# Kernel optimization log

Hardware: AMD Instinct MI355X
Metric: run time of the kernel (lower is better)

## Reference

```python
import jax, jax.numpy as jnp
import numpy as np

B, Q, P = 8, 300, 5
RS, QS, CS, NC = 256, 768, 768, 396
HW = [64, 32, 16, 8]
POOL = [32, 16, 8, 4]
THR = 0.2


def _ln(x, g, b, eps=1e-5):
    m = x.mean(-1, keepdims=True)
    v = ((x - m) ** 2).mean(-1, keepdims=True)
    return (x - m) / jnp.sqrt(v + eps) * g + b


def _avgpool(x, oh, ow):
    # exact adaptive avg pool (output divides input)
    b, c, h, w = x.shape
    return x.reshape(b, c, oh, h // oh, ow, w // ow).mean((3, 5))


def setup_inputs() -> dict:
    key = jax.random.key(0)
    ks = jax.random.split(key, 40)
    inp = {}
    inp['pred_logits'] = jax.random.normal(ks[0], (B, Q, P), dtype=jnp.float32)
    inp['pred_boxes'] = jax.random.uniform(ks[1], (B, Q, 4), dtype=jnp.float32)
    inp['hs'] = jax.random.normal(ks[2], (B, Q, RS), dtype=jnp.float32)
    for s in range(4):
        inp[f'feat{s}'] = jax.random.normal(ks[3 + s], (B, 256, HW[s], HW[s]), dtype=jnp.float32)
        inp[f'pos{s}'] = jax.random.normal(ks[7 + s], (B, 256, HW[s], HW[s]), dtype=jnp.float32)
        inp[f'mask{s}'] = jax.random.bernoulli(ks[11 + s], 0.15, (B, HW[s], HW[s]))
        inp[f'convW{s}'] = jax.random.normal(ks[15 + s], (CS, 256), dtype=jnp.float32) * 0.02
        inp[f'convb{s}'] = jnp.zeros((CS,), jnp.float32)
        inp[f'lng{s}'] = jnp.ones((CS,), jnp.float32)
        inp[f'lnb{s}'] = jnp.zeros((CS,), jnp.float32)
    inp['learnable_query'] = jax.random.normal(ks[19], (P + 1, QS), dtype=jnp.float32)
    inp['Wq'] = jax.random.normal(ks[20], (RS, QS), dtype=jnp.float32) * 0.02
    inp['bq'] = jnp.zeros((QS,), jnp.float32)
    inp['qng'] = jnp.ones((QS,), jnp.float32)
    inp['qnb'] = jnp.zeros((QS,), jnp.float32)
    inp['W1'] = jax.random.normal(ks[21], (QS, QS), dtype=jnp.float32) * 0.02
    inp['b1'] = jnp.zeros((QS,), jnp.float32)
    inp['W2'] = jax.random.normal(ks[22], (QS, NC), dtype=jnp.float32) * 0.02
    inp['b2'] = jnp.zeros((NC,), jnp.float32)
    return inp


def _forward(pred_logits, pred_boxes, hs,
             feats, poss, masks, convWs, convbs, lngs, lnbs,
             learnable_query, Wq, bq, qng, qnb, W1, b1, W2, b2):
    del pred_boxes  # selected in the original but never used
    b = hs.shape[0]
    prob = jax.nn.sigmoid(pred_logits)                       # (B,Q,P)
    # per-prompt membership: logit_i > thr (implies max > thr)
    m = (prob > THR).astype(hs.dtype)                        # (B,Q,P)
    cnt = m.sum(1)                                           # (B,P)
    ssum = jnp.einsum('bqp,bqd->bpd', m, hs)                 # segment-sum over queries
    pooled = jnp.where(cnt[..., None] > 0,
                       ssum / jnp.maximum(cnt, 1.0)[..., None], 0.0)  # (B,P,RS)
    proj = pooled @ Wq + bq                                  # (B,P,QS)
    any_sel = jnp.any(prob.max(-1) > THR, axis=1)            # (B,)
    # if no query passed the global gate, prompt_hs is zeros WITHOUT projection
    prompt_hs = jnp.where(any_sel[:, None, None], proj, 0.0)
    prompt_query = learnable_query[1:] + prompt_hs           # (B,P,QS)
    cls_query = jnp.broadcast_to(learnable_query[0][None, None, :], (b, 1, QS))
    query_tokens = jnp.concatenate([cls_query, prompt_query], axis=1)
    query_tokens = _ln(query_tokens, qng, qnb)               # (B,P+1,QS)

    tokens = []
    for s in range(4):
        mask_f = masks[s][:, None, :, :].astype(feats[s].dtype)   # (B,1,H,W)
        x = (feats[s] + poss[s]) * (1.0 - mask_f)                 # masked_fill
        ctx = jnp.einsum('bchw,oc->bohw', x, convWs[s]) + convbs[s][None, :, None, None]
        p = _avgpool(ctx, POOL[s], POOL[s])
        mp = jnp.clip(_avgpool(1.0 - mask_f, POOL[s], POOL[s]), 1e-6, None)
        p = p / mp
        t = p.reshape(b, CS, -1).transpose(0, 2, 1)               # (B,T_s,CS)
        tokens.append(_ln(t, lngs[s], lnbs[s]))
    ctx_all = jnp.concatenate(tokens, axis=1)                     # (B,1360,CS)

    # encoder stand-in: fuse context into query tokens additively
    last = query_tokens + ctx_all.mean(1)[:, None, :]
    cls_logit = last[:, 0]
    prompt_logit = last[:, 1:].mean(1)
    h = jax.nn.relu((cls_logit + prompt_logit) @ W1 + b1)
    return h @ W2 + b2                                            # (B,NC)


def reference(pred_logits, pred_boxes, hs,
              feat0, pos0, mask0, convW0, convb0, lng0, lnb0,
              feat1, pos1, mask1, convW1, convb1, lng1, lnb1,
              feat2, pos2, mask2, convW2, convb2, lng2, lnb2,
              feat3, pos3, mask3, convW3, convb3, lng3, lnb3,
              learnable_query, Wq, bq, qng, qnb, W1, b1, W2, b2):
    return _forward(pred_logits, pred_boxes, hs,
                    [feat0, feat1, feat2, feat3],
                    [pos0, pos1, pos2, pos3],
                    [mask0, mask1, mask2, mask3],
                    [convW0, convW1, convW2, convW3],
                    [convb0, convb1, convb2, convb3],
                    [lng0, lng1, lng2, lng3],
                    [lnb0, lnb1, lnb2, lnb3],
                    learnable_query, Wq, bq, qng, qnb, W1, b1, W2, b2)
```

## Files before the change

kernel.cpp:

```cpp
#include <hip/hip_runtime.h>
#include <hip/hip_bf16.h>

#define Bn 8
#define Qn 300
#define Pn 5
#define RSn 256
#define QSn 768
#define NCn 396
#define MTOT 10880
#define THRL -1.3862943611198906f

typedef __attribute__((ext_vector_type(8))) short short8;
typedef __attribute__((ext_vector_type(4))) float float4v;

__device__ inline float wred(float v){
  #pragma unroll
  for (int off = 32; off; off >>= 1) v += __shfl_xor(v, off);
  return v;
}

__device__ __forceinline__ unsigned short f2bf(float f){
  union { float f; unsigned int u; } c; c.f = f;
  return (unsigned short)((c.u + 0x7FFF + ((c.u >> 16) & 1)) >> 16);
}

__global__ __launch_bounds__(256, 4) void k_front(
    const float* cw0, const float* cw1, const float* cw2, const float* cw3,
    short* Wswz, const int* __restrict__ mk0, int* det,
    const float* __restrict__ pl, const float* __restrict__ hs,
    float* pooled, int* flags, float* ctxsum, float* outz){
  int bx = blockIdx.x;
  int t = threadIdx.x;
  if (bx < 768){
    int s = bx / 192;
    int linear = (bx % 192)*256 + t;
    int q = linear & 63, n = linear >> 6;
    const float* src = (s==0)?cw0:(s==1)?cw1:(s==2)?cw2:cw3;
    float4 f = *(const float4*)(src + (size_t)n*256 + q*4);
    int kc = q >> 3, lk = (q >> 1) & 3, e0 = (q & 1)*4;
    short* dst = Wswz + ((size_t)(s*8 + kc))*24576 + lk*6144 + n*8 + e0;
    short4 sv;
    sv.x = (short)f2bf(f.x); sv.y = (short)f2bf(f.y);
    sv.z = (short)f2bf(f.z); sv.w = (short)f2bf(f.w);
    *(short4*)dst = sv;
    return;
  }
  if (bx == 768){
    __shared__ int r0[4], r1[4];
    const int* mm = mk0 + t*32;
    int d0 = 0, d1 = 0;
    #pragma unroll 8
    for (int i = 0; i < 32; ++i){
      int v = mm[i];
      d0 |= (v != 0 && v != 1);
      d1 |= (v != 0 && v != 0x3F800000);
    }
    unsigned long long bal0 = __ballot(d0), bal1 = __ballot(d1);
    int wid = t >> 6;
    if ((t & 63) == 0){ r0[wid] = (bal0 != 0ull); r1[wid] = (bal1 != 0ull); }
    __syncthreads();
    if (t == 0){
      det[0] = r0[0] | r0[1] | r0[2] | r0[3];
      det[1] = r1[0] | r1[1] | r1[2] | r1[3];
    }
    return;
  }
  if (bx >= 821){
    int idx = ((bx - 821)*256 + t)*4;
    if (idx < Bn*NCn) *(float4*)(outz + idx) = (float4){0.f,0.f,0.f,0.f};
    return;
  }
  if (bx >= 809){
    int idx = ((bx - 809)*256 + t)*4;
    *(float4*)(ctxsum + idx) = (float4){0.f,0.f,0.f,0.f};
    return;
  }
  __shared__ float msk[Qn];
  int bb = (bx - 769) / Pn, p = (bx - 769) % Pn;
  for (int q = t; q < Qn; q += 256)
    msk[q] = (pl[(bb*Qn + q)*Pn + p] > THRL) ? 1.f : 0.f;
  __syncthreads();
  const float* hb = hs + (size_t)bb*Qn*RSn + t;
  float sA[12];
  #pragma unroll
  for (int i = 0; i < 12; ++i) sA[i] = 0.f;
  float cnt = 0.f;
  for (int q0 = 0; q0 < Qn; q0 += 12){
    #pragma unroll
    for (int i = 0; i < 12; ++i){
      float m = msk[q0 + i];
      cnt += m;
      sA[i] = fmaf(m, hb[(size_t)(q0 + i)*RSn], sA[i]);
    }
  }
  float ssum = ((sA[0]+sA[1]) + (sA[2]+sA[3])) + ((sA[4]+sA[5]) + (sA[6]+sA[7]))
             + ((sA[8]+sA[9]) + (sA[10]+sA[11]));
  pooled[(bb*Pn + p)*RSn + t] = (cnt > 0.f) ? ssum / cnt : 0.f;
  if (t == 0) flags[bb*Pn + p] = (cnt > 0.f) ? 1 : 0;
}

__global__ __launch_bounds__(256, 3) void k_pgemm(
    const float* fe0, const float* po0, const void* ma0,
    const float* fe1, const float* po1, const void* ma1,
    const float* fe2, const float* po2, const void* ma2,
    const float* fe3, const float* po3, const void* ma3,
    const int* __restrict__ det, const short* __restrict__ Wswz,
    const float* cb0, const float* cb1, const float* cb2, const float* cb3,
    const float* lg0, const float* lb0, const float* lg1, const float* lb1,
    const float* lg2, const float* lb2, const float* lg3, const float* lb3,
    float* __restrict__ ctxsum,
    const float* __restrict__ lq, const float* __restrict__ Wq,
    const float* __restrict__ bq, const float* __restrict__ qng,
    const float* __restrict__ qnb, const float* __restrict__ pooled,
    const int* __restrict__ flags, float* qt){
  __shared__ short As[16*264];
  __shared__ float wls[16][4];
  __shared__ float scls[16], imls[16];
  __shared__ float lsum[4][16], lsq[4][16];
  __shared__ float pq[256];
  __shared__ float s1s[4], s2s[4];
  int blk = blockIdx.x;
  int t = threadIdx.x;

  if (blk >= 680){
    int qbx = blk - 680;
    int b = qbx / 6, j = qbx % 6;
    float v0 = lq[j*QSn + t], v1 = lq[j*QSn + t + 256], v2 = lq[j*QSn + t + 512];
    int any = flags[b*Pn] | flags[b*Pn+1] | flags[b*Pn+2] | flags[b*Pn+3] | flags[b*Pn+4];
    if (j > 0 && any){
      pq[t] = pooled[(b*Pn + (j-1))*RSn + t];
      __syncthreads();
      float a0 = 0.f, a1 = 0.f, a2 = 0.f;
      #pragma unroll 8
      for (int c = 0; c < RSn; ++c){
        float pv = pq[c];
        a0 = fmaf(pv, Wq[c*QSn + t      ], a0);
        a1 = fmaf(pv, Wq[c*QSn + t + 256], a1);
        a2 = fmaf(pv, Wq[c*QSn + t + 512], a2);
      }
      v0 += a0 + bq[t]; v1 += a1 + bq[t+256]; v2 += a2 + bq[t+512];
    }
    float sm = v0 + v1 + v2, sq = v0*v0 + v1*v1 + v2*v2;
    sm = wred(sm); sq = wred(sq);
    int wid = t >> 6, lane = t & 63;
    if (lane == 0){ s1s[wid] = sm; s2s[wid] = sq; }
    __syncthreads();
    float S  = s1s[0] + s1s[1] + s1s[2] + s1s[3];
    float SQ = s2s[0] + s2s[1] + s2s[2] + s2s[3];
    float mu = S * (1.f/QSn), var = SQ * (1.f/QSn) - mu*mu;
    float rs = rsqrtf(var + 1e-5f);
    float* o = qt + (b*6 + j)*QSn;
    o[t      ] = (v0 - mu)*rs*qng[t      ] + qnb[t      ];
    o[t + 256] = (v1 - mu)*rs*qng[t + 256] + qnb[t + 256];
    o[t + 512] = (v2 - mu)*rs*qng[t + 512] + qnb[t + 512];
    return;
  }

  int m0 = blk * 16;
  int s, H, OWlog, b0;
  const float *F, *Pp; const void* M;
  const float *CB, *LG, *LB;
  if (m0 < 8192){ s=0; F=fe0; Pp=po0; M=ma0; H=64; OWlog=5; b0=m0>>10;
                  CB=cb0; LG=lg0; LB=lb0; }
  else if (m0 < 10240){ s=1; F=fe1; Pp=po1; M=ma1; H=32; OWlog=4; b0=(m0-8192)>>8;
                  CB=cb1; LG=lg1; LB=lb1; }
  else if (m0 < 10752){ s=2; F=fe2; Pp=po2; M=ma2; H=16; OWlog=3; b0=(m0-10240)>>6;
                  CB=cb2; LG=lg2; LB=lb2; }
  else { s=3; F=fe3; Pp=po3; M=ma3; H=8; OWlog=2; b0=(m0-10752)>>4;
                  CB=cb3; LG=lg3; LB=lb3; }
  int HH = H*H;
  int OWm = (H >> 1) - 1;
  int mode = (det[0] == 0) ? 0 : ((det[1] == 0) ? 2 : 1);

  int slot = t & 15;
  int gm = m0 + slot;
  int bb = b0;
  int ltl;
  if (s == 0)      ltl = gm & 1023;
  else if (s == 1) ltl = gm & 255;
  else if (s == 2) ltl = gm & 63;
  else             ltl = gm & 15;
  int ph = ltl >> OWlog, pw = ltl & OWm;
  int i00 = ph*2*H + pw*2;
  int mbase = bb*HH;

  if (t < 16){
    float w0, w1, w2, w3;
    if (mode == 0){
      const int* Mi = (const int*)M + mbase + i00;
      int2 ma = *(const int2*)(Mi);
      int2 mb = *(const int2*)(Mi + H);
      w0 = ma.x?0.f:1.f; w1 = ma.y?0.f:1.f; w2 = mb.x?0.f:1.f; w3 = mb.y?0.f:1.f;
    } else if (mode == 1){
      const unsigned char* Mb = (const unsigned char*)M + mbase + i00;
      w0 = Mb[0]?0.f:1.f; w1 = Mb[1]?0.f:1.f; w2 = Mb[H]?0.f:1.f; w3 = Mb[H+1]?0.f:1.f;
    } else {
      const float* Mf = (const float*)M + mbase + i00;
      float2 ma = *(const float2*)(Mf);
      float2 mb = *(const float2*)(Mf + H);
      w0 = 1.f-ma.x; w1 = 1.f-ma.y; w2 = 1.f-mb.x; w3 = 1.f-mb.y;
    }
    float msum = w0 + w1 + w2 + w3;
    float im = 1.f / fmaxf(msum*0.25f, 1e-6f);
    wls[t][0] = w0; wls[t][1] = w1; wls[t][2] = w2; wls[t][3] = w3;
    scls[t] = 0.25f*im; imls[t] = im;
  }
  __syncthreads();

  {
    float w0 = wls[slot][0], w1 = wls[slot][1], w2 = wls[slot][2], w3 = wls[slot][3];
    float sc = scls[slot];
    int chb = (t >> 4) * 2;
    size_t base = (size_t)(bb*256 + chb)*HH + i00;
    const float* Fp = F + base;
    const float* Pq = Pp + base;
    const int stride = 32*HH;
    #pragma unroll 2
    for (int r = 0; r < 8; ++r){
      float2 fa0 = *(const float2*)(Fp);
      float2 fb0 = *(const float2*)(Fp + H);
      float2 pa0 = *(const float2*)(Pq);
      float2 pb0 = *(const float2*)(Pq + H);
      float2 fa1 = *(const float2*)(Fp + HH);
      float2 fb1 = *(const float2*)(Fp + HH + H);
      float2 pa1 = *(const float2*)(Pq + HH);
      float2 pb1 = *(const float2*)(Pq + HH + H);
      float x0 = (fa0.x+pa0.x)*w0 + (fa0.y+pa0.y)*w1 + (fb0.x+pb0.x)*w2 + (fb0.y+pb0.y)*w3;
      float x1 = (fa1.x+pa1.x)*w0 + (fa1.y+pa1.y)*w1 + (fb1.x+pb1.x)*w2 + (fb1.y+pb1.y)*w3;
      *(unsigned int*)(&As[slot*264 + chb + r*32]) =
          (unsigned int)f2bf(x0*sc) | ((unsigned int)f2bf(x1*sc) << 16);
      Fp += stride; Pq += stride;
    }
  }
  __syncthreads();

  int wid = t >> 6, l = t & 63;
  int lm = l & 15, lk = l >> 4;
  int nfb = wid * 12;
  short8 aReg[8];
  #pragma unroll
  for (int kc = 0; kc < 8; ++kc)
    aReg[kc] = *(const short8*)(As + lm*264 + kc*32 + lk*8);

  float4v acc[12];
  #pragma unroll
  for (int nf = 0; nf < 12; ++nf) acc[nf] = (float4v){0.f,0.f,0.f,0.f};

  const short* Bb = Wswz + ((size_t)(s*8))*24576 + lk*6144 + nfb*128 + lm*8;
  #pragma unroll
  for (int kc = 0; kc < 8; ++kc){
    const short* bp = Bb + kc*24576;
    #pragma unroll
    for (int nf = 0; nf < 12; ++nf){
      short8 bf = *(const short8*)(bp + nf*128);
      acc[nf] = __builtin_amdgcn_mfma_f32_16x16x32_bf16(aReg[kc], bf, acc[nf], 0, 0, 0);
    }
  }

  float im4[4];
  #pragma unroll
  for (int r = 0; r < 4; ++r) im4[r] = imls[lk*4 + r];

  float sum[4] = {0,0,0,0}, sq[4] = {0,0,0,0};
  #pragma unroll
  for (int nf = 0; nf < 12; ++nf){
    float cbv = CB[(nfb+nf)*16 + lm];
    #pragma unroll
    for (int r = 0; r < 4; ++r){
      float p = acc[nf][r] + cbv*im4[r];
      acc[nf][r] = p;
      sum[r] += p;
      sq[r] = fmaf(p, p, sq[r]);
    }
  }
  #pragma unroll
  for (int r = 0; r < 4; ++r){
    #pragma unroll
    for (int off = 1; off < 16; off <<= 1){
      sum[r] += __shfl_xor(sum[r], off);
      sq[r]  += __shfl_xor(sq[r],  off);
    }
  }
  if (lm == 0){
    #pragma unroll
    for (int r = 0; r < 4; ++r){
      lsum[wid][lk*4 + r] = sum[r];
      lsq[wid][lk*4 + r]  = sq[r];
    }
  }
  __syncthreads();
  float mu[4], rs[4];
  #pragma unroll
  for (int r = 0; r < 4; ++r){
    int row = lk*4 + r;
    float S  = lsum[0][row] + lsum[1][row] + lsum[2][row] + lsum[3][row];
    float SQ = lsq[0][row]  + lsq[1][row]  + lsq[2][row]  + lsq[3][row];
    mu[r] = S * (1.f/768.f);
    float var = SQ * (1.f/768.f) - mu[r]*mu[r];
    rs[r] = rsqrtf(var + 1e-5f);
  }
  #pragma unroll
  for (int nf = 0; nf < 12; ++nf){
    int n = (nfb+nf)*16 + lm;
    float g = LG[n], bv = LB[n];
    float tv = 0.f;
    #pragma unroll
    for (int r = 0; r < 4; ++r)
      tv += (acc[nf][r] - mu[r]) * rs[r];
    tv = tv*g + 4.f*bv;
    tv += __shfl_xor(tv, 16); tv += __shfl_xor(tv, 32);
    if (lk == 0)
      atomicAdd(&ctxsum[b0*768 + n], tv);
  }
}

__global__ void k_hpre(const float* __restrict__ qt, const float* __restrict__ ctxsum,
                       const float* __restrict__ W1, const float* __restrict__ b1,
                       float* __restrict__ hpre){
  __shared__ float vsh[Bn][192];
  int nc = blockIdx.x % 24, kc = blockIdx.x / 24;
  int n0 = nc*32, c0 = kc*192;
  int t = threadIdx.x;
  for (int i = t; i < Bn*192; i += 256){
    int b = i / 192, cl = i - b*192;
    int c = c0 + cl;
    const float* q = qt + (size_t)b*6*768;
    float pm = q[768+c] + q[2*768+c] + q[3*768+c] + q[4*768+c] + q[5*768+c];
    vsh[b][cl] = q[c] + 0.2f*pm + ctxsum[b*768 + c]*(1.f/680.f);
  }
  __syncthreads();
  int ow = t & 31, bi = t >> 5;
  int o = n0 + ow;
  const float* w = W1 + (size_t)c0*768 + o;
  float pacc[16];
  #pragma unroll
  for (int i = 0; i < 16; ++i) pacc[i] = 0.f;
  for (int cl = 0; cl < 192; cl += 16){
    #pragma unroll
    for (int i = 0; i < 16; ++i)
      pacc[i] = fmaf(vsh[bi][cl + i], w[(size_t)(cl + i)*768], pacc[i]);
  }
  float acc = ((pacc[0]+pacc[1])+(pacc[2]+pacc[3])) + ((pacc[4]+pacc[5])+(pacc[6]+pacc[7]))
            + ((pacc[8]+pacc[9])+(pacc[10]+pacc[11])) + ((pacc[12]+pacc[13])+(pacc[14]+pacc[15]));
  if (kc == 0) acc += b1[o];
  atomicAdd(&hpre[bi*768 + o], acc);
}

__global__ void k_out(const float* __restrict__ hpre, const float* __restrict__ W2,
                      const float* __restrict__ b2, float* __restrict__ out){
  __shared__ float hsh[Bn][192];
  int nc = blockIdx.x % 13, kc = blockIdx.x / 13;
  int n0 = nc*32, c0 = kc*192;
  int t = threadIdx.x;
  for (int i = t; i < Bn*192; i += 256){
    int b = i / 192, cl = i - b*192;
    hsh[b][cl] = fmaxf(hpre[b*768 + c0 + cl], 0.f);
  }
  __syncthreads();
  int ow = t & 31, bi = t >> 5;
  int o = n0 + ow;
  if (o >= NCn) return;
  const float* w = W2 + (size_t)c0*NCn + o;
  float pacc[16];
  #pragma unroll
  for (int i = 0; i < 16; ++i) pacc[i] = 0.f;
  for (int cl = 0; cl < 192; cl += 16){
    #pragma unroll
    for (int i = 0; i < 16; ++i)
      pacc[i] = fmaf(hsh[bi][cl + i], w[(size_t)(cl + i)*NCn], pacc[i]);
  }
  float acc = ((pacc[0]+pacc[1])+(pacc[2]+pacc[3])) + ((pacc[4]+pacc[5])+(pacc[6]+pacc[7]))
            + ((pacc[8]+pacc[9])+(pacc[10]+pacc[11])) + ((pacc[12]+pacc[13])+(pacc[14]+pacc[15]));
  if (kc == 0) acc += b2[o];
  atomicAdd(&out[bi*NCn + o], acc);
}

extern "C" void kernel_launch(void* const* d_in, const int* in_sizes, int n_in,
                              void* d_out, int out_size, void* d_ws, size_t ws_size,
                              hipStream_t stream){
  const float* pl = (const float*)d_in[0];
  const float* hs = (const float*)d_in[2];
  const float* feat[4]; const float* pos[4]; const void* mask[4];
  const float* cw[4]; const float* cb[4]; const float* lg[4]; const float* lb[4];
  for (int s = 0; s < 4; ++s){
    int base = 3 + 7*s;
    feat[s] = (const float*)d_in[base];
    pos[s]  = (const float*)d_in[base+1];
    mask[s] = d_in[base+2];
    cw[s]   = (const float*)d_in[base+3];
    cb[s]   = (const float*)d_in[base+4];
    lg[s]   = (const float*)d_in[base+5];
    lb[s]   = (const float*)d_in[base+6];
  }
  const float* lq  = (const float*)d_in[31];
  const float* Wq  = (const float*)d_in[32];
  const float* bq  = (const float*)d_in[33];
  const float* qng = (const float*)d_in[34];
  const float* qnb = (const float*)d_in[35];
  const float* W1  = (const float*)d_in[36];
  const float* b1  = (const float*)d_in[37];
  const float* W2  = (const float*)d_in[38];
  const float* b2  = (const float*)d_in[39];
  float* out = (float*)d_out;

  short* Wswz   = (short*)d_ws;
  float* pooled = (float*)(Wswz + (size_t)4*8*4*768*8);
  float* qt     = pooled + 40*RSn;
  float* ctxsum = qt + Bn*6*QSn;
  float* hpre   = ctxsum + Bn*QSn;
  int*   det    = (int*)(hpre + Bn*QSn);
  int*   flags  = det + 4;

  k_front<<<825, 256, 0, stream>>>(cw[0], cw[1], cw[2], cw[3], Wswz,
                                   (const int*)mask[0], det, pl, hs, pooled, flags,
                                   ctxsum, out);
  k_pgemm<<<728, 256, 0, stream>>>(feat[0], pos[0], mask[0],
                                   feat[1], pos[1], mask[1],
                                   feat[2], pos[2], mask[2],
                                   feat[3], pos[3], mask[3],
                                   det, Wswz,
                                   cb[0], cb[1], cb[2], cb[3],
                                   lg[0], lb[0], lg[1], lb[1],
                                   lg[2], lb[2], lg[3], lb[3], ctxsum,
                                   lq, Wq, bq, qng, qnb, pooled, flags, qt);
  k_hpre<<<96, 256, 0, stream>>>(qt, ctxsum, W1, b1, hpre);
  k_out<<<52, 256, 0, stream>>>(hpre, W2, b2, out);
}
```

Baseline: 242.2 us.

## Shrink pooled-GEMM tiles to 8 rows with 128 threads and float4 loads

The pooled conv-projection kernel now handles 8 pooled positions per block with 2 waves instead of 16 positions with 4 waves, doubling the grid. Each thread computes two adjacent pooled outputs from float4 feature and pos loads, and the mask is read in-thread, which removes a shared-memory stage and one barrier. Block indices are permuted so neighbouring blocks cover interleaved position pairs. The MFMA still runs on 16-row tiles, so half the rows are padding. This duplicates LayerNorm work, makes each wave hold 24 accumulators (more register pressure), and doubles the weight reads and atomics per output row.

```diff
diff --git a/kernel.cpp b/kernel.cpp
--- a/kernel.cpp
+++ b/kernel.cpp
@@ -99,7 +99,7 @@
   if (t == 0) flags[bb*Pn + p] = (cnt > 0.f) ? 1 : 0;
 }
 
-__global__ __launch_bounds__(256, 3) void k_pgemm(
+__global__ __launch_bounds__(128, 2) void k_pgemm(
     const float* fe0, const float* po0, const void* ma0,
     const float* fe1, const float* po1, const void* ma1,
     const float* fe2, const float* po2, const void* ma2,
@@ -114,49 +114,67 @@
     const float* __restrict__ qnb, const float* __restrict__ pooled,
     const int* __restrict__ flags, float* qt){
   __shared__ short As[16*264];
-  __shared__ float wls[16][4];
-  __shared__ float scls[16], imls[16];
-  __shared__ float lsum[4][16], lsq[4][16];
+  __shared__ float imls[8];
+  __shared__ float lsum[2][16], lsq[2][16];
   __shared__ float pq[256];
-  __shared__ float s1s[4], s2s[4];
-  int blk = blockIdx.x;
+  __shared__ float s1s[2], s2s[2];
+  int pblk = blockIdx.x;
   int t = threadIdx.x;
 
-  if (blk >= 680){
-    int qbx = blk - 680;
+  if (pblk >= 1360){
+    int qbx = pblk - 1360;
     int b = qbx / 6, j = qbx % 6;
-    float v0 = lq[j*QSn + t], v1 = lq[j*QSn + t + 256], v2 = lq[j*QSn + t + 512];
+    float v0 = lq[j*QSn + t      ];
+    float v1 = lq[j*QSn + t + 128];
+    float v2 = lq[j*QSn + t + 256];
+    float v3 = lq[j*QSn + t + 384];
+    float v4 = lq[j*QSn + t + 512];
+    float v5 = lq[j*QSn + t + 640];
     int any = flags[b*Pn] | flags[b*Pn+1] | flags[b*Pn+2] | flags[b*Pn+3] | flags[b*Pn+4];
     if (j > 0 && any){
-      pq[t] = pooled[(b*Pn + (j-1))*RSn + t];
+      pq[t      ] = pooled[(b*Pn + (j-1))*RSn + t      ];
+      pq[t + 128] = pooled[(b*Pn + (j-1))*RSn + t + 128];
       __syncthreads();
-      float a0 = 0.f, a1 = 0.f, a2 = 0.f;
+      float a0=0.f,a1=0.f,a2=0.f,a3=0.f,a4=0.f,a5=0.f;
       #pragma unroll 8
       for (int c = 0; c < RSn; ++c){
         float pv = pq[c];
-        a0 = fmaf(pv, Wq[c*QSn + t      ], a0);
-        a1 = fmaf(pv, Wq[c*QSn + t + 256], a1);
-        a2 = fmaf(pv, Wq[c*QSn + t + 512], a2);
+        const float* wr = Wq + c*QSn + t;
+        a0 = fmaf(pv, wr[0],   a0);
+        a1 = fmaf(pv, wr[128], a1);
+        a2 = fmaf(pv, wr[256], a2);
+        a3 = fmaf(pv, wr[384], a3);
+        a4 = fmaf(pv, wr[512], a4);
+        a5 = fmaf(pv, wr[640], a5);
       }
-      v0 += a0 + bq[t]; v1 += a1 + bq[t+256]; v2 += a2 + bq[t+512];
-    }
-    float sm = v0 + v1 + v2, sq = v0*v0 + v1*v1 + v2*v2;
+      v0 += a0 + bq[t];       v1 += a1 + bq[t+128];
+      v2 += a2 + bq[t+256];   v3 += a3 + bq[t+384];
+      v4 += a4 + bq[t+512];   v5 += a5 + bq[t+640];
+    }
+    float sm = (v0+v1) + (v2+v3) + (v4+v5);
+    float sq = (v0*v0+v1*v1) + (v2*v2+v3*v3) + (v4*v4+v5*v5);
     sm = wred(sm); sq = wred(sq);
     int wid = t >> 6, lane = t & 63;
     if (lane == 0){ s1s[wid] = sm; s2s[wid] = sq; }
     __syncthreads();
-    float S  = s1s[0] + s1s[1] + s1s[2] + s1s[3];
-    float SQ = s2s[0] + s2s[1] + s2s[2] + s2s[3];
+    float S  = s1s[0] + s1s[1];
+    float SQ = s2s[0] + s2s[1];
     float mu = S * (1.f/QSn), var = SQ * (1.f/QSn) - mu*mu;
     float rs = rsqrtf(var + 1e-5f);
     float* o = qt + (b*6 + j)*QSn;
     o[t      ] = (v0 - mu)*rs*qng[t      ] + qnb[t      ];
-    o[t + 256] = (v1 - mu)*rs*qng[t + 256] + qnb[t + 256];
-    o[t + 512] = (v2 - mu)*rs*qng[t + 512] + qnb[t + 512];
+    o[t + 128] = (v1 - mu)*rs*qng[t + 128] + qnb[t + 128];
+    o[t + 256] = (v2 - mu)*rs*qng[t + 256] + qnb[t + 256];
+    o[t + 384] = (v3 - mu)*rs*qng[t + 384] + qnb[t + 384];
+    o[t + 512] = (v4 - mu)*rs*qng[t + 512] + qnb[t + 512];
+    o[t + 640] = (v5 - mu)*rs*qng[t + 640] + qnb[t + 640];
     return;
   }
 
-  int m0 = blk * 16;
+  int q16 = pblk >> 4, jj = pblk & 15;
+  int blk = (q16 << 4) + ((jj & 7) << 1) + (jj >> 3);
+
+  int m0 = blk * 8;
   int s, H, OWlog, b0;
   const float *F, *Pp; const void* M;
   const float *CB, *LG, *LB;
@@ -172,86 +190,83 @@
   int OWm = (H >> 1) - 1;
   int mode = (det[0] == 0) ? 0 : ((det[1] == 0) ? 2 : 1);
 
-  int slot = t & 15;
-  int gm = m0 + slot;
-  int bb = b0;
+  int slotp = t & 3;
+  int mA = m0 + slotp*2;
   int ltl;
-  if (s == 0)      ltl = gm & 1023;
-  else if (s == 1) ltl = gm & 255;
-  else if (s == 2) ltl = gm & 63;
-  else             ltl = gm & 15;
+  if (s == 0)      ltl = mA & 1023;
+  else if (s == 1) ltl = mA & 255;
+  else if (s == 2) ltl = mA & 63;
+  else             ltl = mA & 15;
   int ph = ltl >> OWlog, pw = ltl & OWm;
   int i00 = ph*2*H + pw*2;
-  int mbase = bb*HH;
-
-  if (t < 16){
-    float w0, w1, w2, w3;
-    if (mode == 0){
-      const int* Mi = (const int*)M + mbase + i00;
-      int2 ma = *(const int2*)(Mi);
-      int2 mb = *(const int2*)(Mi + H);
-      w0 = ma.x?0.f:1.f; w1 = ma.y?0.f:1.f; w2 = mb.x?0.f:1.f; w3 = mb.y?0.f:1.f;
-    } else if (mode == 1){
-      const unsigned char* Mb = (const unsigned char*)M + mbase + i00;
-      w0 = Mb[0]?0.f:1.f; w1 = Mb[1]?0.f:1.f; w2 = Mb[H]?0.f:1.f; w3 = Mb[H+1]?0.f:1.f;
-    } else {
-      const float* Mf = (const float*)M + mbase + i00;
-      float2 ma = *(const float2*)(Mf);
-      float2 mb = *(const float2*)(Mf + H);
-      w0 = 1.f-ma.x; w1 = 1.f-ma.y; w2 = 1.f-mb.x; w3 = 1.f-mb.y;
-    }
-    float msum = w0 + w1 + w2 + w3;
-    float im = 1.f / fmaxf(msum*0.25f, 1e-6f);
-    wls[t][0] = w0; wls[t][1] = w1; wls[t][2] = w2; wls[t][3] = w3;
-    scls[t] = 0.25f*im; imls[t] = im;
-  }
-  __syncthreads();
+  int mbase = b0*HH;
+
+  float w0A,w1A,w2A,w3A, w0B,w1B,w2B,w3B;
+  if (mode == 0){
+    const int* Mi = (const int*)M + mbase + i00;
+    int4 ma = *(const int4*)(Mi);
+    int4 mb = *(const int4*)(Mi + H);
+    w0A = ma.x?0.f:1.f; w1A = ma.y?0.f:1.f; w2A = mb.x?0.f:1.f; w3A = mb.y?0.f:1.f;
+    w0B = ma.z?0.f:1.f; w1B = ma.w?0.f:1.f; w2B = mb.z?0.f:1.f; w3B = mb.w?0.f:1.f;
+  } else if (mode == 1){
+    const unsigned char* Mb = (const unsigned char*)M + mbase + i00;
+    uchar4 av = *(const uchar4*)(Mb);
+    uchar4 bv = *(const uchar4*)(Mb + H);
+    w0A = av.x?0.f:1.f; w1A = av.y?0.f:1.f; w2A = bv.x?0.f:1.f; w3A = bv.y?0.f:1.f;
+    w0B = av.z?0.f:1.f; w1B = av.w?0.f:1.f; w2B = bv.z?0.f:1.f; w3B = bv.w?0.f:1.f;
+  } else {
+    const float* Mf = (const float*)M + mbase + i00;
+    float4 ma = *(const float4*)(Mf);
+    float4 mb = *(const float4*)(Mf + H);
+    w0A = 1.f-ma.x; w1A = 1.f-ma.y; w2A = 1.f-mb.x; w3A = 1.f-mb.y;
+    w0B = 1.f-ma.z; w1B = 1.f-ma.w; w2B = 1.f-mb.z; w3B = 1.f-mb.w;
+  }
+  float msA = w0A+w1A+w2A+w3A, msB = w0B+w1B+w2B+w3B;
+  float imA = 1.f / fmaxf(msA*0.25f, 1e-6f);
+  float imB = 1.f / fmaxf(msB*0.25f, 1e-6f);
+  float scA = 0.25f*imA, scB = 0.25f*imB;
+  if (t < 4){ imls[slotp*2] = imA; imls[slotp*2 + 1] = imB; }
 
   {
-    float w0 = wls[slot][0], w1 = wls[slot][1], w2 = wls[slot][2], w3 = wls[slot][3];
-    float sc = scls[slot];
-    int chb = (t >> 4) * 2;
-    size_t base = (size_t)(bb*256 + chb)*HH + i00;
+    int cg = t >> 2;
+    size_t base = (size_t)(b0*256 + cg)*HH + i00;
     const float* Fp = F + base;
-    const float* Pq = Pp + base;
-    const int stride = 32*HH;
-    #pragma unroll 2
+    const float* Pq2 = Pp + base;
+    const size_t stride = (size_t)32*HH;
+    int rowA = slotp*2*264, rowB = rowA + 264;
+    #pragma unroll
     for (int r = 0; r < 8; ++r){
-      float2 fa0 = *(const float2*)(Fp);
-      float2 fb0 = *(const float2*)(Fp + H);
-      float2 pa0 = *(const float2*)(Pq);
-      float2 pb0 = *(const float2*)(Pq + H);
-      float2 fa1 = *(const float2*)(Fp + HH);
-      float2 fb1 = *(const float2*)(Fp + HH + H);
-      float2 pa1 = *(const float2*)(Pq + HH);
-      float2 pb1 = *(const float2*)(Pq + HH + H);
-      float x0 = (fa0.x+pa0.x)*w0 + (fa0.y+pa0.y)*w1 + (fb0.x+pb0.x)*w2 + (fb0.y+pb0.y)*w3;
-      float x1 = (fa1.x+pa1.x)*w0 + (fa1.y+pa1.y)*w1 + (fb1.x+pb1.x)*w2 + (fb1.y+pb1.y)*w3;
-      *(unsigned int*)(&As[slot*264 + chb + r*32]) =
-          (unsigned int)f2bf(x0*sc) | ((unsigned int)f2bf(x1*sc) << 16);
-      Fp += stride; Pq += stride;
+      float4 f0 = *(const float4*)(Fp);
+      float4 f1 = *(const float4*)(Fp + H);
+      float4 p0 = *(const float4*)(Pq2);
+      float4 p1 = *(const float4*)(Pq2 + H);
+      float xA = (f0.x+p0.x)*w0A + (f0.y+p0.y)*w1A + (f1.x+p1.x)*w2A + (f1.y+p1.y)*w3A;
+      float xB = (f0.z+p0.z)*w0B + (f0.w+p0.w)*w1B + (f1.z+p1.z)*w2B + (f1.w+p1.w)*w3B;
+      As[rowA + cg + r*32] = (short)f2bf(xA*scA);
+      As[rowB + cg + r*32] = (short)f2bf(xB*scB);
+      Fp += stride; Pq2 += stride;
     }
   }
   __syncthreads();
 
   int wid = t >> 6, l = t & 63;
   int lm = l & 15, lk = l >> 4;
-  int nfb = wid * 12;
+  int nfb = wid * 24;
   short8 aReg[8];
   #pragma unroll
   for (int kc = 0; kc < 8; ++kc)
     aReg[kc] = *(const short8*)(As + lm*264 + kc*32 + lk*8);
 
-  float4v acc[12];
-  #pragma unroll
-  for (int nf = 0; nf < 12; ++nf) acc[nf] = (float4v){0.f,0.f,0.f,0.f};
+  float4v acc[24];
+  #pragma unroll
+  for (int nf = 0; nf < 24; ++nf) acc[nf] = (float4v){0.f,0.f,0.f,0.f};
 
   const short* Bb = Wswz + ((size_t)(s*8))*24576 + lk*6144 + nfb*128 + lm*8;
   #pragma unroll
   for (int kc = 0; kc < 8; ++kc){
     const short* bp = Bb + kc*24576;
     #pragma unroll
-    for (int nf = 0; nf < 12; ++nf){
+    for (int nf = 0; nf < 24; ++nf){
       short8 bf = *(const short8*)(bp + nf*128);
       acc[nf] = __builtin_amdgcn_mfma_f32_16x16x32_bf16(aReg[kc], bf, acc[nf], 0, 0, 0);
     }
@@ -259,11 +274,11 @@
 
   float im4[4];
   #pragma unroll
-  for (int r = 0; r < 4; ++r) im4[r] = imls[lk*4 + r];
+  for (int r = 0; r < 4; ++r) im4[r] = imls[(lk*4 + r) & 7];
 
   float sum[4] = {0,0,0,0}, sq[4] = {0,0,0,0};
   #pragma unroll
-  for (int nf = 0; nf < 12; ++nf){
+  for (int nf = 0; nf < 24; ++nf){
     float cbv = CB[(nfb+nf)*16 + lm];
     #pragma unroll
     for (int r = 0; r < 4; ++r){
@@ -293,14 +308,14 @@
   #pragma unroll
   for (int r = 0; r < 4; ++r){
     int row = lk*4 + r;
-    float S  = lsum[0][row] + lsum[1][row] + lsum[2][row] + lsum[3][row];
-    float SQ = lsq[0][row]  + lsq[1][row]  + lsq[2][row]  + lsq[3][row];
+    float S  = lsum[0][row] + lsum[1][row];
+    float SQ = lsq[0][row]  + lsq[1][row];
     mu[r] = S * (1.f/768.f);
     float var = SQ * (1.f/768.f) - mu[r]*mu[r];
     rs[r] = rsqrtf(var + 1e-5f);
   }
   #pragma unroll
-  for (int nf = 0; nf < 12; ++nf){
+  for (int nf = 0; nf < 24; ++nf){
     int n = (nfb+nf)*16 + lm;
     float g = LG[n], bv = LB[n];
     float tv = 0.f;
@@ -308,6 +323,7 @@
     for (int r = 0; r < 4; ++r)
       tv += (acc[nf][r] - mu[r]) * rs[r];
     tv = tv*g + 4.f*bv;
+    if (lk >= 2) tv = 0.f;
     tv += __shfl_xor(tv, 16); tv += __shfl_xor(tv, 32);
     if (lk == 0)
       atomicAdd(&ctxsum[b0*768 + n], tv);
@@ -414,15 +430,15 @@
   k_front<<<825, 256, 0, stream>>>(cw[0], cw[1], cw[2], cw[3], Wswz,
                                    (const int*)mask[0], det, pl, hs, pooled, flags,
                                    ctxsum, out);
-  k_pgemm<<<728, 256, 0, stream>>>(feat[0], pos[0], mask[0],
-                                   feat[1], pos[1], mask[1],
-                                   feat[2], pos[2], mask[2],
-                                   feat[3], pos[3], mask[3],
-                                   det, Wswz,
-                                   cb[0], cb[1], cb[2], cb[3],
-                                   lg[0], lb[0], lg[1], lb[1],
-                                   lg[2], lb[2], lg[3], lb[3], ctxsum,
-                                   lq, Wq, bq, qng, qnb, pooled, flags, qt);
+  k_pgemm<<<1408, 128, 0, stream>>>(feat[0], pos[0], mask[0],
+                                    feat[1], pos[1], mask[1],
+                                    feat[2], pos[2], mask[2],
+                                    feat[3], pos[3], mask[3],
+                                    det, Wswz,
+                                    cb[0], cb[1], cb[2], cb[3],
+                                    lg[0], lb[0], lg[1], lb[1],
+                                    lg[2], lb[2], lg[3], lb[3], ctxsum,
+                                    lq, Wq, bq, qng, qnb, pooled, flags, qt);
   k_hpre<<<96, 256, 0, stream>>>(qt, ctxsum, W1, b1, hpre);
   k_out<<<52, 256, 0, stream>>>(hpre, W2, b2, out);
 }
```

New measurement: 291.4 us. 20.3% more time.
